# Kernel optimization log

Hardware: AMD Instinct MI355X
Metric: run time of the kernel (lower is better)

## Reference

```python
import jax, jax.numpy as jnp
import numpy as np

D_MODEL = 1024
N_HEADS = 16
D_FF = 4096
EPS = 1e-6


def layer_norm(x, alpha, bias):
    # torch .std default is unbiased (ddof=1)
    mean = jnp.mean(x, axis=-1, keepdims=True)
    std = jnp.std(x, axis=-1, keepdims=True, ddof=1)
    return alpha * (x - mean) / (std + EPS) + bias


def setup_inputs() -> dict:
    key = jax.random.key(0)
    ks = jax.random.split(key, 12)
    B, S, D, H, F = 4, 2048, D_MODEL, N_HEADS, D_FF
    s = 0.02
    return {
        "x": jax.random.normal(ks[0], (B, S, D), dtype=jnp.float32),
        "mask": jnp.ones((1, 1, S, S), dtype=jnp.int32),
        "wq": jax.random.normal(ks[1], (D, D), dtype=jnp.float32) * s,
        "wk": jax.random.normal(ks[2], (D, D), dtype=jnp.float32) * s,
        "wv": jax.random.normal(ks[3], (D, D), dtype=jnp.float32) * s,
        "wo": jax.random.normal(ks[4], (D, D), dtype=jnp.float32) * s,
        "w1": jax.random.normal(ks[5], (D, F), dtype=jnp.float32) * s,
        "b1": jnp.zeros((F,), dtype=jnp.float32),
        "w2": jax.random.normal(ks[6], (F, D), dtype=jnp.float32) * s,
        "b2": jnp.zeros((D,), dtype=jnp.float32),
        "ln1_a": jnp.ones((D,), dtype=jnp.float32),
        "ln1_b": jnp.zeros((D,), dtype=jnp.float32),
        "ln2_a": jnp.ones((D,), dtype=jnp.float32),
        "ln2_b": jnp.zeros((D,), dtype=jnp.float32),
    }


def attention_block(xn, mask, wq, wk, wv, wo):
    B, S, D = xn.shape
    H = N_HEADS
    dk = D // H
    q = (xn @ wq).reshape(B, S, H, dk).transpose(0, 2, 1, 3)  # [B,H,S,dk]
    k = (xn @ wk).reshape(B, S, H, dk).transpose(0, 2, 1, 3)
    v = (xn @ wv).reshape(B, S, H, dk).transpose(0, 2, 1, 3)
    scores = jnp.einsum('bhqd,bhkd->bhqk', q, k) / jnp.sqrt(jnp.float32(dk))
    scores = jnp.where(mask == 0, jnp.float32(-1e9), scores)
    # NOTE: faithful to source — no softmax applied before score @ V
    out = jnp.einsum('bhqk,bhkd->bhqd', scores, v)
    out = out.transpose(0, 2, 1, 3).reshape(B, S, D)
    return out @ wo


def reference(x, mask, wq, wk, wv, wo, w1, b1, w2, b2, ln1_a, ln1_b, ln2_a, ln2_b):
    # residual 1: pre-LN attention (dropout=0 / eval mode)
    x = x + attention_block(layer_norm(x, ln1_a, ln1_b), mask, wq, wk, wv, wo)
    # residual 2: pre-LN FFN
    xn = layer_norm(x, ln2_a, ln2_b)
    ffn = jax.nn.relu(xn @ w1 + b1) @ w2 + b2
    return x + ffn
```

## Files before the change

### kernel.cpp

```cpp
#include <hip/hip_runtime.h>
#include <hip/hip_bf16.h>

typedef __hip_bfloat16 bf16;
typedef __attribute__((ext_vector_type(8))) short short8;
typedef __attribute__((ext_vector_type(4))) float floatx4;

#define D_MODEL 1024
#define SEQ     2048
#define BATCH   4
#define ROWS    (BATCH*SEQ)
#define NH      16
#define DK      64
#define DFF     4096

__device__ __forceinline__ float b2f(short s){
    union { float f; unsigned u; } c; c.u = ((unsigned)(unsigned short)s) << 16; return c.f;
}

__device__ __forceinline__ void gl2lds16(const bf16* g, bf16* l){
    __builtin_amdgcn_global_load_lds(
        (const __attribute__((address_space(1))) void*)g,
        (__attribute__((address_space(3))) void*)l,
        16, 0, 0);
}

__global__ __launch_bounds__(256) void ln_kernel(const float* __restrict__ x,
                                                 const float* __restrict__ alpha,
                                                 const float* __restrict__ beta,
                                                 bf16* __restrict__ out){
    int row = blockIdx.x;
    int t = threadIdx.x;
    float4 v = ((const float4*)(x + (size_t)row*D_MODEL))[t];
    float s  = v.x+v.y+v.z+v.w;
    float ss = v.x*v.x + v.y*v.y + v.z*v.z + v.w*v.w;
    #pragma unroll
    for (int o=32; o; o>>=1){ s += __shfl_down(s,o,64); ss += __shfl_down(ss,o,64); }
    __shared__ float red[8];
    __shared__ float mean_s, scl_s;
    int wid = t>>6, lane = t&63;
    if (lane==0){ red[wid]=s; red[4+wid]=ss; }
    __syncthreads();
    if (t==0){
        float S  = red[0]+red[1]+red[2]+red[3];
        float SS = red[4]+red[5]+red[6]+red[7];
        float mean = S * (1.0f/D_MODEL);
        float var  = (SS - (float)D_MODEL*mean*mean) * (1.0f/(D_MODEL-1));
        var = fmaxf(var, 0.0f);
        mean_s = mean;
        scl_s  = 1.0f/(sqrtf(var) + 1e-6f);
    }
    __syncthreads();
    float mean = mean_s, scl = scl_s;
    float4 a4 = ((const float4*)alpha)[t];
    float4 b4 = ((const float4*)beta)[t];
    bf16 tmp[4];
    tmp[0] = __float2bfloat16(a4.x*((v.x-mean)*scl) + b4.x);
    tmp[1] = __float2bfloat16(a4.y*((v.y-mean)*scl) + b4.y);
    tmp[2] = __float2bfloat16(a4.z*((v.z-mean)*scl) + b4.z);
    tmp[3] = __float2bfloat16(a4.w*((v.w-mean)*scl) + b4.w);
    *(ushort4*)(out + (size_t)row*D_MODEL + t*4) = *(ushort4*)tmp;
}

__global__ __launch_bounds__(256) void cast_transpose(
        const float* __restrict__ wq, const float* __restrict__ wk,
        const float* __restrict__ wv, const float* __restrict__ wo,
        const float* __restrict__ w1, const float* __restrict__ w2,
        bf16* wq_t, bf16* wk_t, bf16* wv_t, bf16* wo_t, bf16* w1_t, bf16* w2_t){
    int b = blockIdx.x;
    const float* src; bf16* dst; int Kd, Nd;
    if      (b < 1024){ src=wq; dst=wq_t; Kd=1024; Nd=1024; }
    else if (b < 2048){ src=wk; dst=wk_t; Kd=1024; Nd=1024; b-=1024; }
    else if (b < 3072){ src=wv; dst=wv_t; Kd=1024; Nd=1024; b-=2048; }
    else if (b < 4096){ src=wo; dst=wo_t; Kd=1024; Nd=1024; b-=3072; }
    else if (b < 8192){ src=w1; dst=w1_t; Kd=1024; Nd=4096; b-=4096; }
    else              { src=w2; dst=w2_t; Kd=4096; Nd=1024; b-=8192; }
    int tilesN = Nd >> 5;
    int kt = b / tilesN, nt = b % tilesN;
    __shared__ float sT[32][33];
    int t = threadIdx.x;
    int tx = t & 31, ty = t >> 5;
    #pragma unroll
    for (int i=0;i<4;i++)
        sT[ty+8*i][tx] = src[(size_t)(kt*32 + ty+8*i)*Nd + nt*32 + tx];
    __syncthreads();
    #pragma unroll
    for (int i=0;i<4;i++){
        int r = ty + 8*i;
        dst[(size_t)(nt*32 + r)*Kd + kt*32 + tx] = __float2bfloat16(sT[tx][r]);
    }
}

template<int EPI>
__global__ __launch_bounds__(256) void gemm128(const bf16* __restrict__ A,
                                               const bf16* __restrict__ Bt,
                                               void* __restrict__ Cout,
                                               const float* __restrict__ bias,
                                               const float* __restrict__ resid,
                                               int K, int N){
    constexpr int BK = 32;
    __shared__ __align__(16) bf16 sA[128*BK];
    __shared__ __align__(16) bf16 sB[128*BK];
    int t = threadIdx.x;
    size_t m0 = (size_t)blockIdx.x * 128, n0 = (size_t)blockIdx.y * 128;
    const bf16* Ab = A  + m0 * K;
    const bf16* Bb = Bt + n0 * K;
    int wid = t >> 6, lane = t & 63;
    int wm = (wid & 1) * 64, wn = (wid >> 1) * 64;
    int fr = lane & 15, quad = lane >> 4;
    floatx4 acc[4][4];
    #pragma unroll
    for (int i=0;i<4;i++)
        #pragma unroll
        for (int j=0;j<4;j++){ floatx4 z = {0.f,0.f,0.f,0.f}; acc[i][j] = z; }

    int c0 = t, c1 = t + 256;
    const bf16* gA0 = Ab + (size_t)(c0 >> 2)*K + (c0 & 3)*8;
    const bf16* gA1 = Ab + (size_t)(c1 >> 2)*K + (c1 & 3)*8;
    const bf16* gB0 = Bb + (size_t)(c0 >> 2)*K + (c0 & 3)*8;
    const bf16* gB1 = Bb + (size_t)(c1 >> 2)*K + (c1 & 3)*8;
    bf16* lA0 = sA + wid*512;
    bf16* lA1 = sA + 2048 + wid*512;
    bf16* lB0 = sB + wid*512;
    bf16* lB1 = sB + 2048 + wid*512;

    for (int k0 = 0; k0 < K; k0 += BK){
        gl2lds16(gA0 + k0, lA0);
        gl2lds16(gA1 + k0, lA1);
        gl2lds16(gB0 + k0, lB0);
        gl2lds16(gB1 + k0, lB1);
        __syncthreads();
        short8 af[4], bfr[4];
        #pragma unroll
        for (int i=0;i<4;i++) af[i]  = *(const short8*)(sA + (wm + i*16 + fr)*BK + quad*8);
        #pragma unroll
        for (int j=0;j<4;j++) bfr[j] = *(const short8*)(sB + (wn + j*16 + fr)*BK + quad*8);
        #pragma unroll
        for (int i=0;i<4;i++)
            #pragma unroll
            for (int j=0;j<4;j++)
                acc[i][j] = __builtin_amdgcn_mfma_f32_16x16x32_bf16(af[i], bfr[j], acc[i][j], 0, 0, 0);
        __syncthreads();
    }

    #pragma unroll
    for (int i=0;i<4;i++){
        #pragma unroll
        for (int j=0;j<4;j++){
            size_t gm = m0 + wm + i*16 + quad*4;
            size_t gn = n0 + wn + j*16 + fr;
            #pragma unroll
            for (int r=0;r<4;r++){
                float v = acc[i][j][r];
                size_t idx = (gm + r) * (size_t)N + gn;
                if constexpr (EPI == 0){
                    ((bf16*)Cout)[idx] = __float2bfloat16(v);
                } else if constexpr (EPI == 1){
                    v += bias[gn]; v = fmaxf(v, 0.0f);
                    ((bf16*)Cout)[idx] = __float2bfloat16(v);
                } else if constexpr (EPI == 2){
                    ((float*)Cout)[idx] = v + resid[idx];
                } else {
                    ((float*)Cout)[idx] = v + bias[gn] + resid[idx];
                }
            }
        }
    }
}

__global__ __launch_bounds__(256) void ktv_partial(const bf16* __restrict__ Kp,
                                                   const bf16* __restrict__ Vp,
                                                   float* __restrict__ ktvp){
    int bx = blockIdx.x;
    int bh = bx >> 3, chunk = bx & 7;
    int b = bh >> 4, h = bh & 15;
    int s_base = chunk * 256;
    __shared__ float sK[32][65], sV[32][65];
    int t = threadIdx.x;
    int ls = t >> 3, lc = (t & 7) * 8;
    int m0 = (t >> 4) * 4, n0 = (t & 15) * 4;
    float acc[4][4] = {};
    for (int ss = 0; ss < 256; ss += 32){
        size_t g = ((size_t)(b*SEQ + s_base + ss + ls))*D_MODEL + h*DK + lc;
        short8 kv = *(const short8*)(Kp + g);
        short8 vv = *(const short8*)(Vp + g);
        #pragma unroll
        for (int e=0;e<8;e++){ sK[ls][lc+e] = b2f(kv[e]); sV[ls][lc+e] = b2f(vv[e]); }
        __syncthreads();
        for (int s=0;s<32;s++){
            float k4[4], v4[4];
            #pragma unroll
            for (int ii=0;ii<4;ii++) k4[ii] = sK[s][m0+ii];
            #pragma unroll
            for (int jj=0;jj<4;jj++) v4[jj] = sV[s][n0+jj];
            #pragma unroll
            for (int ii=0;ii<4;ii++)
                #pragma unroll
                for (int jj=0;jj<4;jj++) acc[ii][jj] += k4[ii]*v4[jj];
        }
        __syncthreads();
    }
    float* outp = ktvp + (size_t)bx * 4096;
    #pragma unroll
    for (int ii=0;ii<4;ii++)
        #pragma unroll
        for (int jj=0;jj<4;jj++) outp[(m0+ii)*64 + n0+jj] = acc[ii][jj];
}

__global__ __launch_bounds__(256) void ktv_reduce(const float* __restrict__ ktvp,
                                                  bf16* __restrict__ ktv){
    int bh = blockIdx.x, t = threadIdx.x;
    for (int e = t; e < 4096; e += 256){
        float s = 0.f;
        #pragma unroll
        for (int c=0;c<8;c++) s += ktvp[((size_t)bh*8 + c)*4096 + e];
        ktv[(size_t)bh*4096 + e] = __float2bfloat16(s * 0.125f);
    }
}

__global__ __launch_bounds__(256) void qktv(const bf16* __restrict__ Q,
                                            const bf16* __restrict__ ktv,
                                            bf16* __restrict__ O){
    int bx = blockIdx.x;
    int bh = bx >> 5, rb = bx & 31;
    int b = bh >> 4, h = bh & 15;
    __shared__ float sQ[64][65], sM[64][65];
    int t = threadIdx.x;
    #pragma unroll
    for (int p=0;p<2;p++){
        int c = t + p*256;
        int row = c >> 3, col = (c & 7) * 8;
        short8 q8 = *(const short8*)(Q + ((size_t)(b*SEQ + rb*64 + row))*D_MODEL + h*DK + col);
        short8 m8 = *(const short8*)(ktv + (size_t)bh*4096 + row*64 + col);
        #pragma unroll
        for (int e=0;e<8;e++){ sQ[row][col+e] = b2f(q8[e]); sM[row][col+e] = b2f(m8[e]); }
    }
    __syncthreads();
    int r0 = (t >> 4) * 4, n0 = (t & 15) * 4;
    float acc[4][4] = {};
    for (int m=0;m<64;m++){
        float q4[4], k4[4];
        #pragma unroll
        for (int ii=0;ii<4;ii++) q4[ii] = sQ[r0+ii][m];
        #pragma unroll
        for (int jj=0;jj<4;jj++) k4[jj] = sM[m][n0+jj];
        #pragma unroll
        for (int ii=0;ii<4;ii++)
            #pragma unroll
            for (int jj=0;jj<4;jj++) acc[ii][jj] += q4[ii]*k4[jj];
    }
    #pragma unroll
    for (int ii=0;ii<4;ii++)
        #pragma unroll
        for (int jj=0;jj<4;jj++)
            O[((size_t)(b*SEQ + rb*64 + r0+ii))*D_MODEL + h*DK + n0+jj] = __float2bfloat16(acc[ii][jj]);
}

extern "C" void kernel_launch(void* const* d_in, const int* in_sizes, int n_in,
                              void* d_out, int out_size, void* d_ws, size_t ws_size,
                              hipStream_t stream){
    const float* x    = (const float*)d_in[0];
    const float* wq   = (const float*)d_in[2];
    const float* wk   = (const float*)d_in[3];
    const float* wv   = (const float*)d_in[4];
    const float* wo   = (const float*)d_in[5];
    const float* w1   = (const float*)d_in[6];
    const float* b1   = (const float*)d_in[7];
    const float* w2   = (const float*)d_in[8];
    const float* b2   = (const float*)d_in[9];
    const float* ln1a = (const float*)d_in[10];
    const float* ln1b = (const float*)d_in[11];
    const float* ln2a = (const float*)d_in[12];
    const float* ln2b = (const float*)d_in[13];

    char* ws = (char*)d_ws;
    const size_t MB = 1024*1024;
    bf16*  wq_t = (bf16*)(ws +   0*MB);
    bf16*  wk_t = (bf16*)(ws +   2*MB);
    bf16*  wv_t = (bf16*)(ws +   4*MB);
    bf16*  wo_t = (bf16*)(ws +   6*MB);
    bf16*  w1_t = (bf16*)(ws +   8*MB);
    bf16*  w2_t = (bf16*)(ws +  16*MB);
    bf16*  xn1  = (bf16*)(ws +  24*MB);
    bf16*  Obuf = xn1;
    bf16*  Qb   = (bf16*)(ws +  40*MB);
    bf16*  xn2  = Qb;
    bf16*  Kb   = (bf16*)(ws +  56*MB);
    bf16*  Vb   = (bf16*)(ws +  72*MB);
    float* ktvp = (float*)(ws +  88*MB);
    bf16*  Hb   = Kb;
    bf16*  ktv  = (bf16*)(ws + 120*MB);
    float* x2   = (float*)(ws + 121*MB);
    float* outp = (float*)d_out;

    dim3 g8(64, 8), g32(64, 32);

    cast_transpose<<<12288, 256, 0, stream>>>(wq, wk, wv, wo, w1, w2,
                                              wq_t, wk_t, wv_t, wo_t, w1_t, w2_t);
    ln_kernel<<<ROWS, 256, 0, stream>>>(x, ln1a, ln1b, xn1);
    gemm128<0><<<g8,  256, 0, stream>>>(xn1, wq_t, Qb, nullptr, nullptr, 1024, 1024);
    gemm128<0><<<g8,  256, 0, stream>>>(xn1, wk_t, Kb, nullptr, nullptr, 1024, 1024);
    gemm128<0><<<g8,  256, 0, stream>>>(xn1, wv_t, Vb, nullptr, nullptr, 1024, 1024);
    ktv_partial<<<512, 256, 0, stream>>>(Kb, Vb, ktvp);
    ktv_reduce<<<64,  256, 0, stream>>>(ktvp, ktv);
    qktv<<<2048, 256, 0, stream>>>(Qb, ktv, Obuf);
    gemm128<2><<<g8,  256, 0, stream>>>(Obuf, wo_t, x2, nullptr, x, 1024, 1024);
    ln_kernel<<<ROWS, 256, 0, stream>>>(x2, ln2a, ln2b, xn2);
    gemm128<1><<<g32, 256, 0, stream>>>(xn2, w1_t, Hb, b1, nullptr, 1024, 4096);
    gemm128<3><<<g8,  256, 0, stream>>>(Hb, w2_t, outp, b2, x2, 4096, 1024);
}
```

Before: 524.9 us.

## Triple-buffer GEMM LDS loads and fuse Q/K/V projections into one GEMM

The bf16 GEMM now keeps three LDS stages filled by global_load_lds and prefetches two k-steps ahead. Each k-step uses a single vmcnt wait plus barrier instead of two __syncthreads, so global loads can overlap with MFMA work. The three Q/K/V projection GEMMs become one N=3072 GEMM that relies on the transposed weights sitting back to back, writing an interleaved QKV buffer that the attention kernels read with a 3072 stride. The extra LDS stages raise LDS use per block, which may limit occupancy. Workspace buffers are also rearranged to fit the larger fused output.

```diff
diff --git a/kernel.cpp b/kernel.cpp
--- a/kernel.cpp
+++ b/kernel.cpp
@@ -12,6 +12,7 @@
 #define NH      16
 #define DK      64
 #define DFF     4096
+#define QKVW    3072
 
 __device__ __forceinline__ float b2f(short s){
     union { float f; unsigned u; } c; c.u = ((unsigned)(unsigned short)s) << 16; return c.f;
@@ -98,8 +99,7 @@
                                                const float* __restrict__ resid,
                                                int K, int N){
     constexpr int BK = 32;
-    __shared__ __align__(16) bf16 sA[128*BK];
-    __shared__ __align__(16) bf16 sB[128*BK];
+    __shared__ __align__(16) bf16 lds[3][2][128*BK];
     int t = threadIdx.x;
     size_t m0 = (size_t)blockIdx.x * 128, n0 = (size_t)blockIdx.y * 128;
     const bf16* Ab = A  + m0 * K;
@@ -118,28 +118,38 @@
     const bf16* gA1 = Ab + (size_t)(c1 >> 2)*K + (c1 & 3)*8;
     const bf16* gB0 = Bb + (size_t)(c0 >> 2)*K + (c0 & 3)*8;
     const bf16* gB1 = Bb + (size_t)(c1 >> 2)*K + (c1 & 3)*8;
-    bf16* lA0 = sA + wid*512;
-    bf16* lA1 = sA + 2048 + wid*512;
-    bf16* lB0 = sB + wid*512;
-    bf16* lB1 = sB + 2048 + wid*512;
+    int o0 = wid*512, o1 = 2048 + wid*512;
+
+    bf16* st0 = &lds[0][0][0];
+    bf16* st1 = &lds[1][0][0];
+    bf16* st2 = &lds[2][0][0];
+
+    gl2lds16(gA0, st0 + o0);  gl2lds16(gA1, st0 + o1);
+    gl2lds16(gB0, st0 + 4096 + o0);  gl2lds16(gB1, st0 + 4096 + o1);
+    gl2lds16(gA0 + BK, st1 + o0);  gl2lds16(gA1 + BK, st1 + o1);
+    gl2lds16(gB0 + BK, st1 + 4096 + o0);  gl2lds16(gB1 + BK, st1 + 4096 + o1);
 
     for (int k0 = 0; k0 < K; k0 += BK){
-        gl2lds16(gA0 + k0, lA0);
-        gl2lds16(gA1 + k0, lA1);
-        gl2lds16(gB0 + k0, lB0);
-        gl2lds16(gB1 + k0, lB1);
-        __syncthreads();
+        if (k0 + BK < K) asm volatile("s_waitcnt vmcnt(4)\n\ts_barrier" ::: "memory");
+        else             asm volatile("s_waitcnt vmcnt(0)\n\ts_barrier" ::: "memory");
+        if (k0 + 2*BK < K){
+            int ka = k0 + 2*BK;
+            gl2lds16(gA0 + ka, st2 + o0);  gl2lds16(gA1 + ka, st2 + o1);
+            gl2lds16(gB0 + ka, st2 + 4096 + o0);  gl2lds16(gB1 + ka, st2 + 4096 + o1);
+        }
+        const bf16* sAc = st0;
+        const bf16* sBc = st0 + 4096;
         short8 af[4], bfr[4];
         #pragma unroll
-        for (int i=0;i<4;i++) af[i]  = *(const short8*)(sA + (wm + i*16 + fr)*BK + quad*8);
-        #pragma unroll
-        for (int j=0;j<4;j++) bfr[j] = *(const short8*)(sB + (wn + j*16 + fr)*BK + quad*8);
+        for (int i=0;i<4;i++) af[i]  = *(const short8*)(sAc + (wm + i*16 + fr)*BK + quad*8);
+        #pragma unroll
+        for (int j=0;j<4;j++) bfr[j] = *(const short8*)(sBc + (wn + j*16 + fr)*BK + quad*8);
         #pragma unroll
         for (int i=0;i<4;i++)
             #pragma unroll
             for (int j=0;j<4;j++)
                 acc[i][j] = __builtin_amdgcn_mfma_f32_16x16x32_bf16(af[i], bfr[j], acc[i][j], 0, 0, 0);
-        __syncthreads();
+        bf16* tmp = st0; st0 = st1; st1 = st2; st2 = tmp;
     }
 
     #pragma unroll
@@ -167,8 +177,7 @@
     }
 }
 
-__global__ __launch_bounds__(256) void ktv_partial(const bf16* __restrict__ Kp,
-                                                   const bf16* __restrict__ Vp,
+__global__ __launch_bounds__(256) void ktv_partial(const bf16* __restrict__ QKV,
                                                    float* __restrict__ ktvp){
     int bx = blockIdx.x;
     int bh = bx >> 3, chunk = bx & 7;
@@ -180,9 +189,9 @@
     int m0 = (t >> 4) * 4, n0 = (t & 15) * 4;
     float acc[4][4] = {};
     for (int ss = 0; ss < 256; ss += 32){
-        size_t g = ((size_t)(b*SEQ + s_base + ss + ls))*D_MODEL + h*DK + lc;
-        short8 kv = *(const short8*)(Kp + g);
-        short8 vv = *(const short8*)(Vp + g);
+        size_t g = ((size_t)(b*SEQ + s_base + ss + ls))*QKVW + h*DK + lc;
+        short8 kv = *(const short8*)(QKV + g + 1024);
+        short8 vv = *(const short8*)(QKV + g + 2048);
         #pragma unroll
         for (int e=0;e<8;e++){ sK[ls][lc+e] = b2f(kv[e]); sV[ls][lc+e] = b2f(vv[e]); }
         __syncthreads();
@@ -217,7 +226,7 @@
     }
 }
 
-__global__ __launch_bounds__(256) void qktv(const bf16* __restrict__ Q,
+__global__ __launch_bounds__(256) void qktv(const bf16* __restrict__ QKV,
                                             const bf16* __restrict__ ktv,
                                             bf16* __restrict__ O){
     int bx = blockIdx.x;
@@ -229,7 +238,7 @@
     for (int p=0;p<2;p++){
         int c = t + p*256;
         int row = c >> 3, col = (c & 7) * 8;
-        short8 q8 = *(const short8*)(Q + ((size_t)(b*SEQ + rb*64 + row))*D_MODEL + h*DK + col);
+        short8 q8 = *(const short8*)(QKV + ((size_t)(b*SEQ + rb*64 + row))*QKVW + h*DK + col);
         short8 m8 = *(const short8*)(ktv + (size_t)bh*4096 + row*64 + col);
         #pragma unroll
         for (int e=0;e<8;e++){ sQ[row][col+e] = b2f(q8[e]); sM[row][col+e] = b2f(m8[e]); }
@@ -280,31 +289,25 @@
     bf16*  wo_t = (bf16*)(ws +   6*MB);
     bf16*  w1_t = (bf16*)(ws +   8*MB);
     bf16*  w2_t = (bf16*)(ws +  16*MB);
-    bf16*  xn1  = (bf16*)(ws +  24*MB);
+    bf16*  QKV  = (bf16*)(ws +  24*MB);
+    bf16*  Hb   = (bf16*)(ws +  24*MB);
+    bf16*  xn1  = (bf16*)(ws +  72*MB);
     bf16*  Obuf = xn1;
-    bf16*  Qb   = (bf16*)(ws +  40*MB);
-    bf16*  xn2  = Qb;
-    bf16*  Kb   = (bf16*)(ws +  56*MB);
-    bf16*  Vb   = (bf16*)(ws +  72*MB);
     float* ktvp = (float*)(ws +  88*MB);
-    bf16*  Hb   = Kb;
-    bf16*  ktv  = (bf16*)(ws + 120*MB);
-    float* x2   = (float*)(ws + 121*MB);
+    bf16*  ktv  = (bf16*)(ws +  96*MB);
+    float* x2   = (float*)(ws +  97*MB);
+    bf16*  xn2  = (bf16*)(ws + 129*MB);
     float* outp = (float*)d_out;
-
-    dim3 g8(64, 8), g32(64, 32);
 
     cast_transpose<<<12288, 256, 0, stream>>>(wq, wk, wv, wo, w1, w2,
                                               wq_t, wk_t, wv_t, wo_t, w1_t, w2_t);
     ln_kernel<<<ROWS, 256, 0, stream>>>(x, ln1a, ln1b, xn1);
-    gemm128<0><<<g8,  256, 0, stream>>>(xn1, wq_t, Qb, nullptr, nullptr, 1024, 1024);
-    gemm128<0><<<g8,  256, 0, stream>>>(xn1, wk_t, Kb, nullptr, nullptr, 1024, 1024);
-    gemm128<0><<<g8,  256, 0, stream>>>(xn1, wv_t, Vb, nullptr, nullptr, 1024, 1024);
-    ktv_partial<<<512, 256, 0, stream>>>(Kb, Vb, ktvp);
+    gemm128<0><<<dim3(64,24), 256, 0, stream>>>(xn1, wq_t, QKV, nullptr, nullptr, 1024, QKVW);
+    ktv_partial<<<512, 256, 0, stream>>>(QKV, ktvp);
     ktv_reduce<<<64,  256, 0, stream>>>(ktvp, ktv);
-    qktv<<<2048, 256, 0, stream>>>(Qb, ktv, Obuf);
-    gemm128<2><<<g8,  256, 0, stream>>>(Obuf, wo_t, x2, nullptr, x, 1024, 1024);
+    qktv<<<2048, 256, 0, stream>>>(QKV, ktv, Obuf);
+    gemm128<2><<<dim3(64,8),  256, 0, stream>>>(Obuf, wo_t, x2, nullptr, x, 1024, 1024);
     ln_kernel<<<ROWS, 256, 0, stream>>>(x2, ln2a, ln2b, xn2);
-    gemm128<1><<<g32, 256, 0, stream>>>(xn2, w1_t, Hb, b1, nullptr, 1024, 4096);
-    gemm128<3><<<g8,  256, 0, stream>>>(Hb, w2_t, outp, b2, x2, 4096, 1024);
-}
+    gemm128<1><<<dim3(64,32), 256, 0, stream>>>(xn2, w1_t, Hb, b1, nullptr, 1024, 4096);
+    gemm128<3><<<dim3(64,8),  256, 0, stream>>>(Hb, w2_t, outp, b2, x2, 4096, 1024);
+}
```

After: 462.4 us. 1.14x faster.
